# Kernel tuning notes

Hardware: AMD Instinct MI355X
Metric: run time of the kernel (lower is better)

Reference implementation:

```python
import jax, jax.numpy as jnp
import numpy as np


def _delta(x, window):
    # x: [B, T, D]; edge-replicate pad by `window` frames on each side,
    # then weighted antisymmetric finite difference: sum_j (x[t+j]-x[t-j])/(2j).
    B, T, D = x.shape
    pad = jnp.concatenate(
        [jnp.repeat(x[:, :1, :], window, axis=1), x, jnp.repeat(x[:, -1:, :], window, axis=1)],
        axis=1,
    )  # [B, T+2W, D]
    z = jnp.zeros_like(x)
    for j in range(1, window + 1):  # tiny fixed loop over window taps
        z = z + (pad[:, window + j: window + j + T, :] - pad[:, window - j: window - j + T, :]) / (2.0 * j)
    return z


def setup_inputs() -> dict:
    key = jax.random.key(0)
    inp = jax.random.normal(key, (32, 4096, 256), dtype=jnp.float32)
    return {"inp": inp, "window": 2}


def reference(inp, window):
    delta = _delta(inp, window)
    double_delta = _delta(delta, window)
    return jnp.concatenate([inp, delta, double_delta], axis=2)  # [B, T, 3D]
```

## Files before the change

### kernel.cpp

```cpp
#include <hip/hip_runtime.h>


#define TT 4096
#define DD 256
#define D4 64
#define O4 192

__device__ __forceinline__ float4 dcomb(const float4 p1, const float4 m1,
                                        const float4 p2, const float4 m2) {
    float4 r;
    r.x = (p1.x - m1.x) * 0.5f + (p2.x - m2.x) * 0.25f;
    r.y = (p1.y - m1.y) * 0.5f + (p2.y - m2.y) * 0.25f;
    r.z = (p1.z - m1.z) * 0.5f + (p2.z - m2.z) * 0.25f;
    r.w = (p1.w - m1.w) * 0.5f + (p2.w - m2.w) * 0.25f;
    return r;
}

__device__ __forceinline__ int clampT(int s) {
    return s < 0 ? 0 : (s > TT - 1 ? TT - 1 : s);
}

__global__ __launch_bounds__(256) void delta_layer_kernel(
        const float* __restrict__ x, float* __restrict__ out, int nthreads) {
    int idx = blockIdx.x * 256 + threadIdx.x;
    if (idx >= nthreads) return;
    int d4 = idx & (D4 - 1);
    int bt = idx >> 6;
    int t  = bt & (TT - 1);
    int b  = bt >> 12;

    const float4* xrow = reinterpret_cast<const float4*>(x)
                         + (long)b * TT * D4 + d4;

    float4 xt, Dm2, Dm1, D0, Dp1, Dp2;

    if (t >= 4 && t <= TT - 5) {
        float4 xa[9];
        #pragma unroll
        for (int k = 0; k < 9; ++k) xa[k] = xrow[(long)(t - 4 + k) * D4];
        xt  = xa[4];
        Dm2 = dcomb(xa[3], xa[1], xa[4], xa[0]);
        Dm1 = dcomb(xa[4], xa[2], xa[5], xa[1]);
        D0  = dcomb(xa[5], xa[3], xa[6], xa[2]);
        Dp1 = dcomb(xa[6], xa[4], xa[7], xa[3]);
        Dp2 = dcomb(xa[7], xa[5], xa[8], xa[4]);
    } else {
        auto X = [&](int s) -> float4 { return xrow[(long)clampT(s) * D4]; };
        auto Dat = [&](int r) -> float4 {
            return dcomb(X(r + 1), X(r - 1), X(r + 2), X(r - 2));
        };
        xt  = X(t);
        D0  = Dat(t);
        Dm2 = Dat(clampT(t - 2));
        Dm1 = Dat(clampT(t - 1));
        Dp1 = Dat(clampT(t + 1));
        Dp2 = Dat(clampT(t + 2));
    }

    float4 dd = dcomb(Dp1, Dm1, Dp2, Dm2);

    float4* o = reinterpret_cast<float4*>(out) + (long)bt * O4 + d4;
    o[0]        = xt;
    o[D4]       = D0;
    o[2 * D4]   = dd;
}

extern "C" void kernel_launch(void* const* d_in, const int* in_sizes, int n_in,
                              void* d_out, int out_size, void* d_ws, size_t ws_size,
                              hipStream_t stream) {
    const float* x = (const float*)d_in[0];
    float* out = (float*)d_out;
    int n_elem = in_sizes[0];
    int nthreads = n_elem / 4;
    int blocks = (nthreads + 255) / 256;
    delta_layer_kernel<<<blocks, 256, 0, stream>>>(x, out, nthreads);
}
```

Baseline: 492.9 us.

## Stream each thread over a run of time steps with register sliding window

Each thread now processes a run of consecutive time steps instead of one, keeping the last five input rows and five first-order deltas in registers and loading only one new row per step. This removes the roughly 9x redundant input loads per output row that relied on cache hits, at the cost of fewer threads and less parallelism, since the thread count drops by the run length. The end-of-sequence clamp for deltas is handled by repeating the last delta, and the per-thread bounds guard was removed.

```diff
diff --git a/kernel.cpp b/kernel.cpp
--- a/kernel.cpp
+++ b/kernel.cpp
@@ -1,10 +1,10 @@
 #include <hip/hip_runtime.h>
 
 
-#define TT 4096
-#define DD 256
-#define D4 64
-#define O4 192
+#define TT   4096
+#define D4   64
+#define O4   192
+#define TRUN 32
 
 __device__ __forceinline__ float4 dcomb(const float4 p1, const float4 m1,
                                         const float4 p2, const float4 m2) {
@@ -21,48 +21,48 @@
 }
 
 __global__ __launch_bounds__(256) void delta_layer_kernel(
-        const float* __restrict__ x, float* __restrict__ out, int nthreads) {
+        const float* __restrict__ x, float* __restrict__ out) {
     int idx = blockIdx.x * 256 + threadIdx.x;
-    if (idx >= nthreads) return;
-    int d4 = idx & (D4 - 1);
-    int bt = idx >> 6;
-    int t  = bt & (TT - 1);
-    int b  = bt >> 12;
+    int d4  = idx & (D4 - 1);
+    int seg = idx >> 6;
+    int t0  = (seg & (TT / TRUN - 1)) * TRUN;
+    int b   = seg >> 7;
 
-    const float4* xrow = reinterpret_cast<const float4*>(x)
-                         + (long)b * TT * D4 + d4;
+    const float4* xb = reinterpret_cast<const float4*>(x) + b * TT * D4 + d4;
 
-    float4 xt, Dm2, Dm1, D0, Dp1, Dp2;
+    auto ldc = [&](int r) -> float4 { return xb[clampT(r) * D4]; };
+    auto deltaAt = [&](int r) -> float4 {
+        return dcomb(ldc(r + 1), ldc(r - 1), ldc(r + 2), ldc(r - 2));
+    };
 
-    if (t >= 4 && t <= TT - 5) {
-        float4 xa[9];
-        #pragma unroll
-        for (int k = 0; k < 9; ++k) xa[k] = xrow[(long)(t - 4 + k) * D4];
-        xt  = xa[4];
-        Dm2 = dcomb(xa[3], xa[1], xa[4], xa[0]);
-        Dm1 = dcomb(xa[4], xa[2], xa[5], xa[1]);
-        D0  = dcomb(xa[5], xa[3], xa[6], xa[2]);
-        Dp1 = dcomb(xa[6], xa[4], xa[7], xa[3]);
-        Dp2 = dcomb(xa[7], xa[5], xa[8], xa[4]);
-    } else {
-        auto X = [&](int s) -> float4 { return xrow[(long)clampT(s) * D4]; };
-        auto Dat = [&](int r) -> float4 {
-            return dcomb(X(r + 1), X(r - 1), X(r + 2), X(r - 2));
-        };
-        xt  = X(t);
-        D0  = Dat(t);
-        Dm2 = Dat(clampT(t - 2));
-        Dm1 = Dat(clampT(t - 1));
-        Dp1 = Dat(clampT(t + 1));
-        Dp2 = Dat(clampT(t + 2));
+    float4 dm2 = deltaAt(clampT(t0 - 2));
+    float4 dm1 = deltaAt(clampT(t0 - 1));
+    float4 dc  = deltaAt(t0);
+    float4 dp1 = deltaAt(clampT(t0 + 1));
+    float4 dp2 = deltaAt(clampT(t0 + 2));
+    float4 x0 = ldc(t0),     x1 = ldc(t0 + 1), x2 = ldc(t0 + 2);
+    float4 x3 = ldc(t0 + 3), x4 = ldc(t0 + 4);
+
+    float4* ob = reinterpret_cast<float4*>(out) + (b * TT + t0) * O4 + d4;
+
+    #pragma unroll
+    for (int tt = 0; tt < TRUN; ++tt) {
+        int t = t0 + tt;
+        ob[0]      = x0;
+        ob[D4]     = dc;
+        ob[2 * D4] = dcomb(dp1, dm1, dp2, dm2);
+
+        float4 xn = ldc(t + 5);
+        float4 dn;
+        if (t + 3 <= TT - 1) {
+            dn = dcomb(x4, x2, xn, x1);
+        } else {
+            dn = dp2;
+        }
+        dm2 = dm1; dm1 = dc; dc = dp1; dp1 = dp2; dp2 = dn;
+        x0 = x1; x1 = x2; x2 = x3; x3 = x4; x4 = xn;
+        ob += O4;
     }
-
-    float4 dd = dcomb(Dp1, Dm1, Dp2, Dm2);
-
-    float4* o = reinterpret_cast<float4*>(out) + (long)bt * O4 + d4;
-    o[0]        = xt;
-    o[D4]       = D0;
-    o[2 * D4]   = dd;
 }
 
 extern "C" void kernel_launch(void* const* d_in, const int* in_sizes, int n_in,
@@ -70,8 +70,7 @@
                               hipStream_t stream) {
     const float* x = (const float*)d_in[0];
     float* out = (float*)d_out;
-    int n_elem = in_sizes[0];
-    int nthreads = n_elem / 4;
+    int nthreads = (in_sizes[0] / 256 / TRUN) * D4;
     int blocks = (nthreads + 255) / 256;
-    delta_layer_kernel<<<blocks, 256, 0, stream>>>(x, out, nthreads);
+    delta_layer_kernel<<<blocks, 256, 0, stream>>>(x, out);
 }
```

Measured after the change: 491.7 us. Within noise of the previous version (-0.2%).
